# Kernel tuning notes

Measured on AMD Instinct MI355X. Metric: run time of the kernel, lower is better.

## Reference

```python
import jax, jax.numpy as jnp
from jax import lax
import numpy as np

UNITS = 400
FEAT = 3
B, T = 64, 512


def _lstm_layer(x, Wx, Wh, pi, pf, po, b):
    """Peephole LSTM (Graves 2013). x: [B,T,D] -> [B,T,U]."""
    Bsz = x.shape[0]
    U = Wh.shape[0]
    # Precompute input projections for all timesteps: [B,T,4U]
    xproj = jnp.einsum('btd,dk->btk', x, Wx) + b
    xs = jnp.swapaxes(xproj, 0, 1)  # [T,B,4U]

    def step(carry, xp):
        h, c = carry
        z = xp + h @ Wh  # [B,4U]
        zi, zf, zg, zo = jnp.split(z, 4, axis=-1)
        i = jax.nn.sigmoid(zi + pi * c)
        f = jax.nn.sigmoid(zf + pf * c)
        g = jnp.tanh(zg)
        c_new = f * c + i * g
        o = jax.nn.sigmoid(zo + po * c_new)
        h_new = o * jnp.tanh(c_new)
        return (h_new, c_new), h_new

    init = (jnp.zeros((Bsz, U), x.dtype), jnp.zeros((Bsz, U), x.dtype))
    _, hs = lax.scan(step, init, xs)
    return jnp.swapaxes(hs, 0, 1)  # [B,T,U]


def setup_inputs() -> dict:
    key = jax.random.key(0)
    ks = jax.random.split(key, 32)
    ki = iter(range(32))
    s = 0.05
    d = {'x': jax.random.normal(ks[next(ki)], (B, T, FEAT), jnp.float32)}
    in_dims = [FEAT, UNITS, UNITS]
    for l, din in enumerate(in_dims):
        d[f'Wx{l}'] = jax.random.normal(ks[next(ki)], (din, 4 * UNITS), jnp.float32) * s
        d[f'Wh{l}'] = jax.random.normal(ks[next(ki)], (UNITS, 4 * UNITS), jnp.float32) * s
        d[f'pi{l}'] = jax.random.normal(ks[next(ki)], (UNITS,), jnp.float32) * s
        d[f'pf{l}'] = jax.random.normal(ks[next(ki)], (UNITS,), jnp.float32) * s
        d[f'po{l}'] = jax.random.normal(ks[next(ki)], (UNITS,), jnp.float32) * s
        d[f'b{l}'] = jnp.zeros((4 * UNITS,), jnp.float32)
    d['Wd'] = jax.random.normal(ks[next(ki)], (UNITS, FEAT), jnp.float32) * s
    d['bd'] = jnp.zeros((FEAT,), jnp.float32)
    return d


def reference(x, Wx0, Wh0, pi0, pf0, po0, b0,
              Wx1, Wh1, pi1, pf1, po1, b1,
              Wx2, Wh2, pi2, pf2, po2, b2,
              Wd, bd):
    h = _lstm_layer(x, Wx0, Wh0, pi0, pf0, po0, b0)
    h = _lstm_layer(h, Wx1, Wh1, pi1, pf1, po1, b1)
    h = _lstm_layer(h, Wx2, Wh2, pi2, pf2, po2, b2)
    return h @ Wd + bd  # [B,T,FEAT]
```

## Files before the change

### kernel.cpp

```cpp
#include <hip/hip_runtime.h>
#include <math.h>

#define B64   64
#define TT    512
#define U400  400
#define G1600 1600
#define NBPL  80
#define UPB   5
#define NW    8
#define NTHR  512
#define NBLK  (3 * NBPL)

__device__ __forceinline__ float ldg_c(const float* p) {
  return __hip_atomic_load(p, __ATOMIC_RELAXED, __HIP_MEMORY_SCOPE_AGENT);
}
__device__ __forceinline__ void stg_c(float* p, float v) {
  __hip_atomic_store(p, v, __ATOMIC_RELAXED, __HIP_MEMORY_SCOPE_AGENT);
}

__global__ void xpose_x_k(const float* __restrict__ x, float* __restrict__ xT) {
  int idx = blockIdx.x * 256 + threadIdx.x;
  if (idx < B64 * TT * 3) {
    int d = idx % 3;
    int t = (idx / 3) % TT;
    int b = idx / (3 * TT);
    xT[(t * 3 + d) * B64 + b] = x[idx];
  }
}

__global__ void transpose_k(const float* __restrict__ in, float* __restrict__ out,
                            int R, int C) {
  __shared__ float tile[32][33];
  int bx = blockIdx.x * 32, by = blockIdx.y * 32;
  int tx = threadIdx.x, ty = threadIdx.y;
  #pragma unroll
  for (int i = ty; i < 32; i += 8) {
    int r = by + i, c = bx + tx;
    if (r < R && c < C) tile[i][tx] = in[(size_t)r * C + c];
  }
  __syncthreads();
  #pragma unroll
  for (int i = ty; i < 32; i += 8) {
    int r = bx + i, c = by + tx;
    if (r < C && c < R) out[(size_t)r * R + c] = tile[tx][i];
  }
}

struct ScanP {
  const float *xT0, *Wx0;
  const float *WxT1, *WxT2;
  const float *WhT0, *WhT1, *WhT2;
  const float *b0, *b1, *b2;
  const float *pi0, *pi1, *pi2;
  const float *pf0, *pf1, *pf2;
  const float *po0, *po1, *po2;
  float *h0r, *h1r;
  float *h2;
  unsigned *sync;
};

__launch_bounds__(NTHR, 1)
__global__ void lstm_scan_k(ScanP p) {
  const int l    = blockIdx.x / NBPL;
  const int u0   = (blockIdx.x % NBPL) * UPB;
  const int lane = threadIdx.x & 63;
  const int kq   = __builtin_amdgcn_readfirstlane(threadIdx.x >> 6);

  __shared__ float zs[NW][4 * UPB][B64];

  const float* WhT  = (l == 0) ? p.WhT0 : (l == 1 ? p.WhT1 : p.WhT2);
  const float* WxT  = (l == 1) ? p.WxT1 : p.WxT2;
  const float* bias = (l == 0) ? p.b0  : (l == 1 ? p.b1  : p.b2);
  const float* pi   = (l == 0) ? p.pi0 : (l == 1 ? p.pi1 : p.pi2);
  const float* pf   = (l == 0) ? p.pf0 : (l == 1 ? p.pf1 : p.pf2);
  const float* po   = (l == 0) ? p.po0 : (l == 1 ? p.po1 : p.po2);
  const float* prevb = (l == 1) ? p.h0r : p.h1r;
  float* ownb = (l == 0) ? p.h0r : (l == 1 ? p.h1r : p.h2);
  const int ownmask = (l == 2) ? (TT - 1) : 7;

  unsigned* cnt = p.sync;
  unsigned* acc_ = p.sync + 3;

  const float* wb; int k0, klenf, isH;
  if (l == 0)      { wb = WhT; k0 = kq * 50;        klenf = 50;  isH = 1; }
  else if (kq < 4) { wb = WxT; k0 = kq * 100;       klenf = 100; isH = 0; }
  else             { wb = WhT; k0 = (kq - 4) * 100; klenf = 100; isH = 1; }

  const float* wrow[4 * UPB];
  #pragma unroll
  for (int g = 0; g < 4; ++g)
    #pragma unroll
    for (int uu = 0; uu < UPB; ++uu)
      wrow[g * UPB + uu] = wb + (size_t)(g * U400 + u0 + uu) * U400 + k0;

  float creg = 0.f;

  for (int t = 0; t < TT; ++t) {
    if (threadIdx.x == 0) {
      while ((int)__hip_atomic_load(&cnt[l], __ATOMIC_RELAXED,
                                    __HIP_MEMORY_SCOPE_AGENT) < t)
        __builtin_amdgcn_s_sleep(1);
      if (l > 0)
        while ((int)__hip_atomic_load(&cnt[l - 1], __ATOMIC_RELAXED,
                                      __HIP_MEMORY_SCOPE_AGENT) < t + 1)
          __builtin_amdgcn_s_sleep(1);
      if (l < 2)
        while ((int)__hip_atomic_load(&cnt[l + 1], __ATOMIC_RELAXED,
                                      __HIP_MEMORY_SCOPE_AGENT) < t - 7)
          __builtin_amdgcn_s_sleep(1);
    }
    __syncthreads();

    {
      float acc[4 * UPB];
      #pragma unroll
      for (int c = 0; c < 4 * UPB; ++c) acc[c] = 0.f;

      const int klen = (isH && t == 0) ? 0 : klenf;
      if (klen) {
        const float* aslab = isH
            ? ownb  + (size_t)((t - 1) & ownmask) * (U400 * B64) + (size_t)k0 * B64
            : prevb + (size_t)(t & 7)             * (U400 * B64) + (size_t)k0 * B64;
        #pragma unroll 4
        for (int kk = 0; kk < klen; ++kk) {
          float a = ldg_c(&aslab[kk * B64 + lane]);
          #pragma unroll
          for (int c = 0; c < 4 * UPB; ++c) acc[c] += a * wrow[c][kk];
        }
      }
      #pragma unroll
      for (int c = 0; c < 4 * UPB; ++c) zs[kq][c][lane] = acc[c];
    }
    __syncthreads();

    if (threadIdx.x < UPB * B64) {
      const int uu = threadIdx.x >> 6;
      const int b  = lane;
      const int u  = u0 + uu;
      float z0 = bias[0 * U400 + u], z1 = bias[1 * U400 + u];
      float z2 = bias[2 * U400 + u], z3 = bias[3 * U400 + u];
      #pragma unroll
      for (int w = 0; w < NW; ++w) {
        z0 += zs[w][0 * UPB + uu][b];
        z1 += zs[w][1 * UPB + uu][b];
        z2 += zs[w][2 * UPB + uu][b];
        z3 += zs[w][3 * UPB + uu][b];
      }
      if (l == 0) {
        #pragma unroll
        for (int dd = 0; dd < 3; ++dd) {
          float xv = p.xT0[(t * 3 + dd) * B64 + b];
          z0 += xv * p.Wx0[dd * G1600 + 0 * U400 + u];
          z1 += xv * p.Wx0[dd * G1600 + 1 * U400 + u];
          z2 += xv * p.Wx0[dd * G1600 + 2 * U400 + u];
          z3 += xv * p.Wx0[dd * G1600 + 3 * U400 + u];
        }
      }
      float cp = creg;
      float ig = 1.f / (1.f + expf(-(z0 + pi[u] * cp)));
      float fg = 1.f / (1.f + expf(-(z1 + pf[u] * cp)));
      float gg = tanhf(z2);
      float cn = fg * cp + ig * gg;
      float og = 1.f / (1.f + expf(-(z3 + po[u] * cn)));
      creg = cn;
      float h = og * tanhf(cn);
      stg_c(&ownb[(size_t)(t & ownmask) * (U400 * B64) + (size_t)u * B64 + b], h);
    }

    __syncthreads();

    if (threadIdx.x == 0) {
      unsigned old = __hip_atomic_fetch_add(&acc_[l], 1u, __ATOMIC_RELAXED,
                                            __HIP_MEMORY_SCOPE_AGENT);
      if (old == (unsigned)((t + 1) * NBPL - 1))
        __hip_atomic_store(&cnt[l], (unsigned)(t + 1), __ATOMIC_RELAXED,
                           __HIP_MEMORY_SCOPE_AGENT);
    }
  }
}

__launch_bounds__(256)
__global__ void dense_k(const float* __restrict__ h2, const float* __restrict__ Wd,
                        const float* __restrict__ bd, float* __restrict__ out) {
  int wid  = blockIdx.x * 4 + (threadIdx.x >> 6);
  int lane = threadIdx.x & 63;
  int t = wid / 3, f = wid - t * 3;
  if (t >= TT) return;
  float acc = bd[f];
  const float* hrow = h2 + (size_t)t * U400 * B64 + lane;
  #pragma unroll 4
  for (int u = 0; u < U400; ++u) acc += hrow[(size_t)u * B64] * Wd[u * 3 + f];
  out[((size_t)lane * TT + t) * 3 + f] = acc;
}

extern "C" void kernel_launch(void* const* d_in, const int* in_sizes, int n_in,
                              void* d_out, int out_size, void* d_ws, size_t ws_size,
                              hipStream_t stream) {
  const float* x   = (const float*)d_in[0];
  const float* Wx0 = (const float*)d_in[1];
  const float* Wh0 = (const float*)d_in[2];
  const float* pi0 = (const float*)d_in[3];
  const float* pf0 = (const float*)d_in[4];
  const float* po0 = (const float*)d_in[5];
  const float* b0  = (const float*)d_in[6];
  const float* Wx1 = (const float*)d_in[7];
  const float* Wh1 = (const float*)d_in[8];
  const float* pi1 = (const float*)d_in[9];
  const float* pf1 = (const float*)d_in[10];
  const float* po1 = (const float*)d_in[11];
  const float* b1  = (const float*)d_in[12];
  const float* Wx2 = (const float*)d_in[13];
  const float* Wh2 = (const float*)d_in[14];
  const float* pi2 = (const float*)d_in[15];
  const float* pf2 = (const float*)d_in[16];
  const float* po2 = (const float*)d_in[17];
  const float* b2  = (const float*)d_in[18];
  const float* Wd  = (const float*)d_in[19];
  const float* bd  = (const float*)d_in[20];

  float* ws   = (float*)d_ws;
  float* xT0  = ws;
  float* WhT0 = xT0  + 98304;
  float* WhT1 = WhT0 + 640000;
  float* WhT2 = WhT1 + 640000;
  float* WxT1 = WhT2 + 640000;
  float* WxT2 = WxT1 + 640000;
  float* h0r  = WxT2 + 640000;
  float* h1r  = h0r  + 204800;
  float* h2   = h1r  + 204800;
  unsigned* syn = (unsigned*)(h2 + 13107200);

  hipMemsetAsync(syn, 0, 64, stream);

  hipLaunchKernelGGL(xpose_x_k, dim3(384), dim3(256), 0, stream, x, xT0);

  dim3 tb(32, 8);
  dim3 tg((G1600 + 31) / 32, (U400 + 31) / 32);
  hipLaunchKernelGGL(transpose_k, tg, tb, 0, stream, Wh0, WhT0, U400, G1600);
  hipLaunchKernelGGL(transpose_k, tg, tb, 0, stream, Wh1, WhT1, U400, G1600);
  hipLaunchKernelGGL(transpose_k, tg, tb, 0, stream, Wh2, WhT2, U400, G1600);
  hipLaunchKernelGGL(transpose_k, tg, tb, 0, stream, Wx1, WxT1, U400, G1600);
  hipLaunchKernelGGL(transpose_k, tg, tb, 0, stream, Wx2, WxT2, U400, G1600);

  ScanP hp;
  hp.xT0 = xT0;  hp.Wx0 = Wx0;
  hp.WxT1 = WxT1; hp.WxT2 = WxT2;
  hp.WhT0 = WhT0; hp.WhT1 = WhT1; hp.WhT2 = WhT2;
  hp.b0 = b0; hp.b1 = b1; hp.b2 = b2;
  hp.pi0 = pi0; hp.pi1 = pi1; hp.pi2 = pi2;
  hp.pf0 = pf0; hp.pf1 = pf1; hp.pf2 = pf2;
  hp.po0 = po0; hp.po1 = po1; hp.po2 = po2;
  hp.h0r = h0r; hp.h1r = h1r; hp.h2 = h2;
  hp.sync = syn;

  void* args[] = { &hp };
  hipLaunchCooperativeKernel((void*)lstm_scan_k, dim3(NBLK), dim3(NTHR),
                             args, 0, stream);

  hipLaunchKernelGGL(dense_k, dim3(384), dim3(256), 0, stream, h2, Wd, bd,
                     (float*)d_out);
}
```

Before: 18.54 ms.

## Per-wave dependency spinning and double-buffered activation loads in LSTM scan GEMM

Replaces the single-thread spin plus block barrier at the start of each timestep with per-wave waits, so each wave waits only on the counter it depends on. Wx waves wait on the previous layer and Wh waves on their own layer, letting input-projection waves start while recurrent waves are still stalled. The inner GEMM becomes a fully unrolled, chunked loop that prefetches the next 25 activation loads into registers while computing on the current chunk. This aims to hide global-load latency and cut synchronisation stalls, at the cost of more register pressure. The backpressure wait moves to the last wave only.

```diff
diff --git a/kernel.cpp b/kernel.cpp
--- a/kernel.cpp
+++ b/kernel.cpp
@@ -7,6 +7,7 @@
 #define G1600 1600
 #define NBPL  80
 #define UPB   5
+#define NCOL  (4 * UPB)
 #define NW    8
 #define NTHR  512
 #define NBLK  (3 * NBPL)
@@ -16,6 +17,9 @@
 }
 __device__ __forceinline__ void stg_c(float* p, float v) {
   __hip_atomic_store(p, v, __ATOMIC_RELAXED, __HIP_MEMORY_SCOPE_AGENT);
+}
+__device__ __forceinline__ int adl(const unsigned* p) {
+  return (int)__hip_atomic_load(p, __ATOMIC_RELAXED, __HIP_MEMORY_SCOPE_AGENT);
 }
 
 __global__ void xpose_x_k(const float* __restrict__ x, float* __restrict__ xT) {
@@ -43,6 +47,32 @@
   for (int i = ty; i < 32; i += 8) {
     int r = bx + i, c = by + tx;
     if (r < C && c < R) out[(size_t)r * R + c] = tile[tx][i];
+  }
+}
+
+template <int CH, int NCH>
+__device__ __forceinline__ void gemm_slice(const float* __restrict__ aslab,
+                                           int lane,
+                                           const float* const (&wrow)[NCOL],
+                                           float (&acc)[NCOL]) {
+  float buf[2][CH];
+  #pragma unroll
+  for (int i = 0; i < CH; ++i)
+    buf[0][i] = ldg_c(aslab + (size_t)i * B64 + lane);
+  #pragma unroll
+  for (int c = 0; c < NCH; ++c) {
+    if (c + 1 < NCH) {
+      #pragma unroll
+      for (int i = 0; i < CH; ++i)
+        buf[(c + 1) & 1][i] = ldg_c(aslab + (size_t)((c + 1) * CH + i) * B64 + lane);
+    }
+    #pragma unroll
+    for (int i = 0; i < CH; ++i) {
+      const float a = buf[c & 1][i];
+      const int k = c * CH + i;
+      #pragma unroll
+      for (int cc = 0; cc < NCOL; ++cc) acc[cc] += a * wrow[cc][k];
+    }
   }
 }
 
@@ -66,7 +96,7 @@
   const int lane = threadIdx.x & 63;
   const int kq   = __builtin_amdgcn_readfirstlane(threadIdx.x >> 6);
 
-  __shared__ float zs[NW][4 * UPB][B64];
+  __shared__ float zs[NW][NCOL][B64];
 
   const float* WhT  = (l == 0) ? p.WhT0 : (l == 1 ? p.WhT1 : p.WhT2);
   const float* WxT  = (l == 1) ? p.WxT1 : p.WxT2;
@@ -78,15 +108,16 @@
   float* ownb = (l == 0) ? p.h0r : (l == 1 ? p.h1r : p.h2);
   const int ownmask = (l == 2) ? (TT - 1) : 7;
 
-  unsigned* cnt = p.sync;
+  unsigned* cnt  = p.sync;
   unsigned* acc_ = p.sync + 3;
 
-  const float* wb; int k0, klenf, isH;
-  if (l == 0)      { wb = WhT; k0 = kq * 50;        klenf = 50;  isH = 1; }
-  else if (kq < 4) { wb = WxT; k0 = kq * 100;       klenf = 100; isH = 0; }
-  else             { wb = WhT; k0 = (kq - 4) * 100; klenf = 100; isH = 1; }
-
-  const float* wrow[4 * UPB];
+  const float* wb; int k0, isH;
+  if (l == 0)      { wb = WhT; k0 = kq * 50;        isH = 1; }
+  else if (kq < 4) { wb = WxT; k0 = kq * 100;       isH = 0; }
+  else             { wb = WhT; k0 = (kq - 4) * 100; isH = 1; }
+  const bool isWx = (l > 0) && (kq < 4);
+
+  const float* wrow[NCOL];
   #pragma unroll
   for (int g = 0; g < 4; ++g)
     #pragma unroll
@@ -96,40 +127,29 @@
   float creg = 0.f;
 
   for (int t = 0; t < TT; ++t) {
-    if (threadIdx.x == 0) {
-      while ((int)__hip_atomic_load(&cnt[l], __ATOMIC_RELAXED,
-                                    __HIP_MEMORY_SCOPE_AGENT) < t)
-        __builtin_amdgcn_s_sleep(1);
-      if (l > 0)
-        while ((int)__hip_atomic_load(&cnt[l - 1], __ATOMIC_RELAXED,
-                                      __HIP_MEMORY_SCOPE_AGENT) < t + 1)
-          __builtin_amdgcn_s_sleep(1);
-      if (l < 2)
-        while ((int)__hip_atomic_load(&cnt[l + 1], __ATOMIC_RELAXED,
-                                      __HIP_MEMORY_SCOPE_AGENT) < t - 7)
-          __builtin_amdgcn_s_sleep(1);
-    }
-    __syncthreads();
+    if (isWx) {
+      while (adl(&cnt[l - 1]) < t + 1) __builtin_amdgcn_s_sleep(2);
+    } else if (t > 0) {
+      while (adl(&cnt[l]) < t) __builtin_amdgcn_s_sleep(2);
+    }
+    if (l < 2 && kq == NW - 1) {
+      while (adl(&cnt[l + 1]) < t - 7) __builtin_amdgcn_s_sleep(2);
+    }
 
     {
-      float acc[4 * UPB];
-      #pragma unroll
-      for (int c = 0; c < 4 * UPB; ++c) acc[c] = 0.f;
-
-      const int klen = (isH && t == 0) ? 0 : klenf;
-      if (klen) {
+      float acc[NCOL];
+      #pragma unroll
+      for (int c = 0; c < NCOL; ++c) acc[c] = 0.f;
+
+      if (!(isH && t == 0)) {
         const float* aslab = isH
             ? ownb  + (size_t)((t - 1) & ownmask) * (U400 * B64) + (size_t)k0 * B64
             : prevb + (size_t)(t & 7)             * (U400 * B64) + (size_t)k0 * B64;
-        #pragma unroll 4
-        for (int kk = 0; kk < klen; ++kk) {
-          float a = ldg_c(&aslab[kk * B64 + lane]);
-          #pragma unroll
-          for (int c = 0; c < 4 * UPB; ++c) acc[c] += a * wrow[c][kk];
-        }
+        if (l == 0) gemm_slice<25, 2>(aslab, lane, wrow, acc);
+        else        gemm_slice<25, 4>(aslab, lane, wrow, acc);
       }
       #pragma unroll
-      for (int c = 0; c < 4 * UPB; ++c) zs[kq][c][lane] = acc[c];
+      for (int c = 0; c < NCOL; ++c) zs[kq][c][lane] = acc[c];
     }
     __syncthreads();
 
```

Measured after the change: 30.67 ms. +65.4%, slower.
